# Kernel tuning notes

Measured on AMD Instinct MI355X. Metric: run time of the kernel, lower is better.

The kernel has to match this reference:

```python
import jax, jax.numpy as jnp
import numpy as np

EPS = 1e-8

def setup_inputs() -> dict:
    key = jax.random.key(0)
    k1, k2 = jax.random.split(key)
    B, N, M, D = 8, 4096, 4096, 3
    x1 = jax.random.normal(k1, (B, N, D), dtype=jnp.float32)
    y1 = jax.random.normal(k2, (B, M, D), dtype=jnp.float32)
    return {"x1": x1, "y1": y1}

def reference(x1, y1):
    # Faithful to: dist = sqrt(1e-8 + sum((x1[:,None,:,:] - y1[:,:,None,:])**2, -1))
    # computed via the Gram-matrix expansion to avoid the (B,M,N,D) intermediate.
    x_sq = jnp.sum(x1 * x1, axis=-1)                 # (B, N)
    y_sq = jnp.sum(y1 * y1, axis=-1)                 # (B, M)
    xy = jnp.einsum('bmd,bnd->bmn', y1, x1)          # (B, M, N)
    d2 = jnp.maximum(y_sq[:, :, None] + x_sq[:, None, :] - 2.0 * xy, 0.0)
    dist = jnp.sqrt(EPS + d2)                        # (B, M, N)
    min1 = jnp.min(dist, axis=1)                     # (B, N): nearest y for each x
    min2 = jnp.min(dist, axis=2)                     # (B, M): nearest x for each y
    return jnp.mean(min1) + jnp.mean(min2)
```

## Files before the change

kernel.cpp:

```cpp
#include <hip/hip_runtime.h>

constexpr int B = 8;
constexpr int N = 4096;

#define TPB 256
#define R 4
#define CHUNK 256
#define NCHUNK (N / CHUNK)
#define NTILE (N / (TPB * R))

__global__ void init_min(unsigned int* __restrict__ p, int n) {
    int i = blockIdx.x * blockDim.x + threadIdx.x;
    if (i < n) p[i] = 0x7F800000u;
}

__global__ __launch_bounds__(TPB) void chamfer_min2(
        const float* __restrict__ x1,
        const float* __restrict__ y1,
        unsigned int* __restrict__ outbits) {
    __shared__ float4 ys[CHUNK];

    const int dir   = blockIdx.y / NCHUNK;
    const int chunk = blockIdx.y % NCHUNK;
    const int b     = blockIdx.z;
    const int tile  = blockIdx.x;

    const float* own = dir ? y1 : x1;
    const float* oth = dir ? x1 : y1;
    unsigned int* obits = outbits + (size_t)dir * B * N + (size_t)b * N;

    const float* op = oth + ((size_t)b * N + chunk * CHUNK) * 3;
    if (threadIdx.x < CHUNK) {
        int t = threadIdx.x;
        float qx = op[3 * t], qy = op[3 * t + 1], qz = op[3 * t + 2];
        float qq = fmaf(qx, qx, fmaf(qy, qy, qz * qz));
        ys[t] = make_float4(qx, qy, qz, qq);
    }

    const int ibase = tile * (TPB * R) + threadIdx.x;
    float mx[R], my[R], mz[R], xx[R], acc[R];
    #pragma unroll
    for (int r = 0; r < R; r++) {
        const float* pp = own + ((size_t)b * N + ibase + r * TPB) * 3;
        float px = pp[0], py = pp[1], pz = pp[2];
        mx[r] = -2.0f * px; my[r] = -2.0f * py; mz[r] = -2.0f * pz;
        xx[r] = fmaf(px, px, fmaf(py, py, pz * pz));
        acc[r] = 3.4e38f;
    }

    __syncthreads();

    #pragma unroll 4
    for (int j = 0; j < CHUNK; j++) {
        float4 q = ys[j];
        #pragma unroll
        for (int r = 0; r < R; r++) {
            float g = fmaf(mx[r], q.x, fmaf(my[r], q.y, fmaf(mz[r], q.z, q.w)));
            acc[r] = fminf(acc[r], g);
        }
    }

    #pragma unroll
    for (int r = 0; r < R; r++) {
        float d2 = fmaxf(acc[r] + xx[r], 0.0f);
        atomicMin(&obits[ibase + r * TPB], __float_as_uint(d2));
    }
}

__global__ __launch_bounds__(1024) void chamfer_reduce(
        const unsigned int* __restrict__ bits,
        float* __restrict__ out, int total, float scale) {
    float s = 0.0f;
    for (int i = threadIdx.x; i < total; i += 1024) {
        float d2 = __uint_as_float(bits[i]);
        s += sqrtf(1e-8f + d2);
    }
    #pragma unroll
    for (int off = 32; off > 0; off >>= 1) s += __shfl_down(s, off, 64);

    __shared__ float partial[16];
    const int wid = threadIdx.x >> 6, lane = threadIdx.x & 63;
    if (lane == 0) partial[wid] = s;
    __syncthreads();
    if (threadIdx.x < 16) {
        float v = partial[threadIdx.x];
        #pragma unroll
        for (int off = 8; off > 0; off >>= 1) v += __shfl_down(v, off, 16);
        if (threadIdx.x == 0) out[0] = v * scale;
    }
}

extern "C" void kernel_launch(void* const* d_in, const int* in_sizes, int n_in,
                              void* d_out, int out_size, void* d_ws, size_t ws_size,
                              hipStream_t stream) {
    const float* x1 = (const float*)d_in[0];
    const float* y1 = (const float*)d_in[1];
    float* out = (float*)d_out;

    unsigned int* minbits = (unsigned int*)d_ws;
    const int total = 2 * B * N;

    init_min<<<(total + 255) / 256, 256, 0, stream>>>(minbits, total);

    dim3 grid(NTILE, 2 * NCHUNK, B);
    chamfer_min2<<<grid, TPB, 0, stream>>>(x1, y1, minbits);

    chamfer_reduce<<<1, 1024, 0, stream>>>(minbits, out, total, 1.0f / (B * N));
}
```

Baseline: 100.4 us.

## Replace atomicMin with per-chunk partials, precompute query float4s, parallelize final reduce

A prep kernel now precomputes (x,y,z,|q|^2) float4 records for both point sets, so the main kernel stages its shared-memory chunk with one vector load instead of recomputing it. The main kernel writes per-chunk minima to a partials buffer with plain stores instead of global atomicMin. A many-block finish kernel takes the minimum across chunks, applies sqrt and sums into the output with atomicAdd, replacing the single-block reduction. CHUNK is halved, which doubles the grid and the number of partial planes, and adds memory traffic plus a float atomicAdd whose summation order can vary between runs.

```diff
diff --git a/kernel.cpp b/kernel.cpp
--- a/kernel.cpp
+++ b/kernel.cpp
@@ -2,41 +2,44 @@
 
 constexpr int B = 8;
 constexpr int N = 4096;
+constexpr int PTS = B * N;
+constexpr int TOT = 2 * PTS;
 
 #define TPB 256
 #define R 4
-#define CHUNK 256
+#define CHUNK 128
 #define NCHUNK (N / CHUNK)
 #define NTILE (N / (TPB * R))
 
-__global__ void init_min(unsigned int* __restrict__ p, int n) {
-    int i = blockIdx.x * blockDim.x + threadIdx.x;
-    if (i < n) p[i] = 0x7F800000u;
+__global__ __launch_bounds__(256) void prep(
+        const float* __restrict__ x1, const float* __restrict__ y1,
+        float4* __restrict__ qpre, float* __restrict__ out) {
+    int tid = blockIdx.x * 256 + threadIdx.x;
+    if (tid == 0) out[0] = 0.0f;
+    if (tid >= TOT) return;
+    int dir = tid >> 15;
+    int p   = tid & (PTS - 1);
+    const float* src = dir ? x1 : y1;
+    float qx = src[3 * p], qy = src[3 * p + 1], qz = src[3 * p + 2];
+    float qq = fmaf(qx, qx, fmaf(qy, qy, qz * qz));
+    qpre[tid] = make_float4(qx, qy, qz, qq);
 }
 
-__global__ __launch_bounds__(TPB) void chamfer_min2(
-        const float* __restrict__ x1,
-        const float* __restrict__ y1,
-        unsigned int* __restrict__ outbits) {
-    __shared__ float4 ys[CHUNK];
+__global__ __launch_bounds__(TPB) void chamfer_min3(
+        const float* __restrict__ x1, const float* __restrict__ y1,
+        const float4* __restrict__ qpre,
+        float* __restrict__ partials) {
+    __shared__ float4 qs[CHUNK];
 
     const int dir   = blockIdx.y / NCHUNK;
     const int chunk = blockIdx.y % NCHUNK;
     const int b     = blockIdx.z;
     const int tile  = blockIdx.x;
 
+    const float4* qp = qpre + (size_t)dir * PTS + (size_t)b * N + chunk * CHUNK;
+    if (threadIdx.x < CHUNK) qs[threadIdx.x] = qp[threadIdx.x];
+
     const float* own = dir ? y1 : x1;
-    const float* oth = dir ? x1 : y1;
-    unsigned int* obits = outbits + (size_t)dir * B * N + (size_t)b * N;
-
-    const float* op = oth + ((size_t)b * N + chunk * CHUNK) * 3;
-    if (threadIdx.x < CHUNK) {
-        int t = threadIdx.x;
-        float qx = op[3 * t], qy = op[3 * t + 1], qz = op[3 * t + 2];
-        float qq = fmaf(qx, qx, fmaf(qy, qy, qz * qz));
-        ys[t] = make_float4(qx, qy, qz, qq);
-    }
-
     const int ibase = tile * (TPB * R) + threadIdx.x;
     float mx[R], my[R], mz[R], xx[R], acc[R];
     #pragma unroll
@@ -52,7 +55,7 @@
 
     #pragma unroll 4
     for (int j = 0; j < CHUNK; j++) {
-        float4 q = ys[j];
+        float4 q = qs[j];
         #pragma unroll
         for (int r = 0; r < R; r++) {
             float g = fmaf(mx[r], q.x, fmaf(my[r], q.y, fmaf(mz[r], q.z, q.w)));
@@ -60,33 +63,30 @@
         }
     }
 
+    float* dst = partials + (size_t)chunk * TOT + (size_t)dir * PTS + (size_t)b * N;
     #pragma unroll
     for (int r = 0; r < R; r++) {
-        float d2 = fmaxf(acc[r] + xx[r], 0.0f);
-        atomicMin(&obits[ibase + r * TPB], __float_as_uint(d2));
+        dst[ibase + r * TPB] = fmaxf(acc[r] + xx[r], 0.0f);
     }
 }
 
-__global__ __launch_bounds__(1024) void chamfer_reduce(
-        const unsigned int* __restrict__ bits,
-        float* __restrict__ out, int total, float scale) {
-    float s = 0.0f;
-    for (int i = threadIdx.x; i < total; i += 1024) {
-        float d2 = __uint_as_float(bits[i]);
-        s += sqrtf(1e-8f + d2);
-    }
+__global__ __launch_bounds__(256) void chamfer_finish(
+        const float* __restrict__ partials, float* __restrict__ out, float scale) {
+    int p = blockIdx.x * 256 + threadIdx.x;
+    float m = partials[p];
+    #pragma unroll
+    for (int c = 1; c < NCHUNK; c++) m = fminf(m, partials[(size_t)c * TOT + p]);
+    float s = sqrtf(1e-8f + m) * scale;
+
     #pragma unroll
     for (int off = 32; off > 0; off >>= 1) s += __shfl_down(s, off, 64);
 
-    __shared__ float partial[16];
+    __shared__ float partial[4];
     const int wid = threadIdx.x >> 6, lane = threadIdx.x & 63;
     if (lane == 0) partial[wid] = s;
     __syncthreads();
-    if (threadIdx.x < 16) {
-        float v = partial[threadIdx.x];
-        #pragma unroll
-        for (int off = 8; off > 0; off >>= 1) v += __shfl_down(v, off, 16);
-        if (threadIdx.x == 0) out[0] = v * scale;
+    if (threadIdx.x == 0) {
+        atomicAdd(out, partial[0] + partial[1] + partial[2] + partial[3]);
     }
 }
 
@@ -97,13 +97,13 @@
     const float* y1 = (const float*)d_in[1];
     float* out = (float*)d_out;
 
-    unsigned int* minbits = (unsigned int*)d_ws;
-    const int total = 2 * B * N;
+    float4* qpre    = (float4*)d_ws;
+    float* partials = (float*)(qpre + TOT);
 
-    init_min<<<(total + 255) / 256, 256, 0, stream>>>(minbits, total);
+    prep<<<TOT / 256, 256, 0, stream>>>(x1, y1, qpre, out);
 
     dim3 grid(NTILE, 2 * NCHUNK, B);
-    chamfer_min2<<<grid, TPB, 0, stream>>>(x1, y1, minbits);
+    chamfer_min3<<<grid, TPB, 0, stream>>>(x1, y1, qpre, partials);
 
-    chamfer_reduce<<<1, 1024, 0, stream>>>(minbits, out, total, 1.0f / (B * N));
+    chamfer_finish<<<TOT / 256, 256, 0, stream>>>(partials, out, 1.0f / (B * N));
 }
```

Measured after the change: 84.69 us. -15.6%, faster.
